# Optimization experiments

Measured on AMD Instinct MI355X. Metric: run time of the kernel, lower is better.

## Reference

```python
import jax, jax.numpy as jnp
import numpy as np

EMBED = 512
HEADS = 8
HIDDEN = 4 * EMBED
EPS = 1e-5


def setup_inputs() -> dict:
    key = jax.random.key(0)
    ks = jax.random.split(key, 12)
    s = lambda fan_in: 1.0 / np.sqrt(fan_in)
    return {
        "x": jax.random.normal(ks[0], (4, 2048, EMBED), dtype=jnp.float32),
        "ln1_g": jnp.ones((EMBED,), jnp.float32),
        "ln1_b": jnp.zeros((EMBED,), jnp.float32),
        "qkv_w": jax.random.uniform(ks[1], (EMBED, 3 * EMBED), jnp.float32, -s(EMBED), s(EMBED)),
        "qkv_b": jax.random.uniform(ks[2], (3 * EMBED,), jnp.float32, -s(EMBED), s(EMBED)),
        "proj_w": jax.random.uniform(ks[3], (EMBED, EMBED), jnp.float32, -s(EMBED), s(EMBED)),
        "proj_b": jax.random.uniform(ks[4], (EMBED,), jnp.float32, -s(EMBED), s(EMBED)),
        "ln2_g": jnp.ones((EMBED,), jnp.float32),
        "ln2_b": jnp.zeros((EMBED,), jnp.float32),
        "fc1_w": jax.random.uniform(ks[5], (EMBED, HIDDEN), jnp.float32, -s(EMBED), s(EMBED)),
        "fc1_b": jax.random.uniform(ks[6], (HIDDEN,), jnp.float32, -s(EMBED), s(EMBED)),
        "fc2_w": jax.random.uniform(ks[7], (HIDDEN, EMBED), jnp.float32, -s(HIDDEN), s(HIDDEN)),
        "fc2_b": jax.random.uniform(ks[8], (EMBED,), jnp.float32, -s(HIDDEN), s(HIDDEN)),
    }


def _layernorm(x, g, b):
    mu = jnp.mean(x, axis=-1, keepdims=True)
    var = jnp.mean(jnp.square(x - mu), axis=-1, keepdims=True)
    return (x - mu) * jax.lax.rsqrt(var + EPS) * g + b


def reference(x, ln1_g, ln1_b, qkv_w, qkv_b, proj_w, proj_b,
              ln2_g, ln2_b, fc1_w, fc1_b, fc2_w, fc2_b):
    B, N, C = x.shape
    H, D = HEADS, C // HEADS
    scale = D ** -0.5

    # --- attention sub-block (pre-LN) ---
    h = _layernorm(x, ln1_g, ln1_b)
    qkv = h @ qkv_w + qkv_b                      # [B,N,3C]
    q, k, v = jnp.split(qkv, 3, axis=-1)
    q = q.reshape(B, N, H, D).transpose(0, 2, 1, 3)  # [B,H,N,D]
    k = k.reshape(B, N, H, D).transpose(0, 2, 1, 3)
    v = v.reshape(B, N, H, D).transpose(0, 2, 1, 3)
    attn = jnp.einsum('bhqd,bhkd->bhqk', q, k) * scale
    attn = jax.nn.softmax(attn, axis=-1)
    o = jnp.einsum('bhqk,bhkd->bhqd', attn, v)
    o = o.transpose(0, 2, 1, 3).reshape(B, N, C)
    x = x + (o @ proj_w + proj_b)

    # --- MLP sub-block (pre-LN, exact GELU) ---
    h = _layernorm(x, ln2_g, ln2_b)
    h = jax.nn.gelu(h @ fc1_w + fc1_b, approximate=False)
    x = x + (h @ fc2_w + fc2_b)
    return x
```

## Files before the change

### kernel.cpp

```cpp
#include <hip/hip_runtime.h>
#include <math.h>


using bf16x8 = __attribute__((ext_vector_type(8))) short;
using f32x4  = __attribute__((ext_vector_type(4))) float;
using f32x16 = __attribute__((ext_vector_type(16))) float;

typedef unsigned short u16;
typedef unsigned int   u32;

__device__ __forceinline__ u16 f2bf(float f) {
    u32 u; __builtin_memcpy(&u, &f, 4);
    u32 r = u + 0x7FFFu + ((u >> 16) & 1u);
    return (u16)(r >> 16);
}
__device__ __forceinline__ u32 fbits(float f) {
    u32 u; __builtin_memcpy(&u, &f, 4); return u;
}
__device__ __forceinline__ float f_from_bits(u32 u) {
    float f; __builtin_memcpy(&f, &u, 4); return f;
}
__device__ __forceinline__ u32 pack_trunc(float lo, float hi) {
    return __builtin_amdgcn_perm(fbits(hi), fbits(lo), 0x07060302u);
}
__device__ __forceinline__ void gload16(const void* g, void* l) {
    __builtin_amdgcn_global_load_lds(
        (const __attribute__((address_space(1))) unsigned int*)g,
        (__attribute__((address_space(3))) unsigned int*)l, 16, 0, 0);
}

__global__ __launch_bounds__(256) void k_pre(
        const float* __restrict__ w0, u16* __restrict__ d0,
        const float* __restrict__ w1, u16* __restrict__ d1,
        const float* __restrict__ w2, u16* __restrict__ d2,
        const float* __restrict__ w3, u16* __restrict__ d3,
        const float* __restrict__ x, const float* __restrict__ g,
        const float* __restrict__ bta, u16* __restrict__ hout) {
    __shared__ float tile[32][33];
    const int bid = blockIdx.x;
    if (bid < 3072) {
        const float* w; u16* dst; int K, N, tb;
        if (bid < 768)       { w = w0; dst = d0; K = 512;  N = 1536; tb = bid; }
        else if (bid < 1024) { w = w1; dst = d1; K = 512;  N = 512;  tb = bid - 768; }
        else if (bid < 2048) { w = w2; dst = d2; K = 512;  N = 2048; tb = bid - 1024; }
        else                 { w = w3; dst = d3; K = 2048; N = 512;  tb = bid - 2048; }
        const int nb = N >> 5;
        const int k0 = (tb / nb) << 5;
        const int n0 = (tb % nb) << 5;
        const int c = threadIdx.x & 31, r = threadIdx.x >> 5;
#pragma unroll
        for (int i = 0; i < 4; i++)
            tile[r + i * 8][c] = w[(size_t)(k0 + r + i * 8) * N + n0 + c];
        __syncthreads();
#pragma unroll
        for (int i = 0; i < 4; i++)
            dst[(size_t)(n0 + r + i * 8) * K + k0 + c] = f2bf(tile[c][r + i * 8]);
    } else {
        const int row  = ((bid - 3072) << 2) + (threadIdx.x >> 6);
        const int lane = threadIdx.x & 63;
        const float* xr = x + (size_t)row * 512 + lane * 8;
        float4 a = *(const float4*)xr;
        float4 c = *(const float4*)(xr + 4);
        float s = a.x + a.y + a.z + a.w + c.x + c.y + c.z + c.w;
        float q = a.x*a.x + a.y*a.y + a.z*a.z + a.w*a.w
                + c.x*c.x + c.y*c.y + c.z*c.z + c.w*c.w;
#pragma unroll
        for (int off = 32; off; off >>= 1) {
            s += __shfl_xor(s, off, 64);
            q += __shfl_xor(q, off, 64);
        }
        const float mean = s * (1.0f / 512.0f);
        const float var  = q * (1.0f / 512.0f) - mean * mean;
        const float rstd = rsqrtf(var + 1e-5f);
        float vv[8] = {a.x, a.y, a.z, a.w, c.x, c.y, c.z, c.w};
#pragma unroll
        for (int j = 0; j < 8; j++) {
            const int col = lane * 8 + j;
            hout[(size_t)row * 512 + col] = f2bf((vv[j] - mean) * rstd * g[col] + bta[col]);
        }
    }
}

__global__ __launch_bounds__(256) void k_ln(const float* __restrict__ x,
                                            const float* __restrict__ g,
                                            const float* __restrict__ bta,
                                            u16* __restrict__ out) {
    const int row  = (blockIdx.x << 2) + (threadIdx.x >> 6);
    const int lane = threadIdx.x & 63;
    const float* xr = x + (size_t)row * 512 + lane * 8;
    float4 a = *(const float4*)xr;
    float4 c = *(const float4*)(xr + 4);
    float s = a.x + a.y + a.z + a.w + c.x + c.y + c.z + c.w;
    float q = a.x*a.x + a.y*a.y + a.z*a.z + a.w*a.w
            + c.x*c.x + c.y*c.y + c.z*c.z + c.w*c.w;
#pragma unroll
    for (int off = 32; off; off >>= 1) {
        s += __shfl_xor(s, off, 64);
        q += __shfl_xor(q, off, 64);
    }
    const float mean = s * (1.0f / 512.0f);
    const float var  = q * (1.0f / 512.0f) - mean * mean;
    const float rstd = rsqrtf(var + 1e-5f);
    float vv[8] = {a.x, a.y, a.z, a.w, c.x, c.y, c.z, c.w};
#pragma unroll
    for (int j = 0; j < 8; j++) {
        const int col = lane * 8 + j;
        out[(size_t)row * 512 + col] = f2bf((vv[j] - mean) * rstd * g[col] + bta[col]);
    }
}

template <int EP, int TN>
__global__ __launch_bounds__(256, 3) void k_gemm(const u16* __restrict__ A,
                                                 const u16* __restrict__ Bt,
                                                 const float* __restrict__ bias,
                                                 const float* __restrict__ res,
                                                 float* __restrict__ outF,
                                                 u16* __restrict__ outB,
                                                 u16* __restrict__ out2,
                                                 int M, int N, int K) {
    constexpr int NT = TN / 32;
    __shared__ u16 As[128 * 64];
    __shared__ u16 Bs[TN * 64];
    const int nb = N / TN;
    const int xg = blockIdx.x & 7, sg = blockIdx.x >> 3;
    const int m0 = ((sg / nb) * 8 + xg) << 7;
    const int n0 = (sg % nb) * TN;
    const int t = threadIdx.x, lane = t & 63, w = t >> 6;
    const int wr = (w >> 1) << 6;
    const int wc = (w & 1) * (TN / 2);
    const int quad = lane >> 4, l15 = lane & 15;
    const int x7 = l15 & 7;

    f32x4 acc[4][NT];
#pragma unroll
    for (int i = 0; i < 4; i++)
#pragma unroll
        for (int j = 0; j < NT; j++) acc[i][j] = (f32x4){0.f, 0.f, 0.f, 0.f};

    const size_t Kb = (size_t)K * 2;
    const char* ga = (const char*)A + (size_t)m0 * Kb;
    const char* gb = (const char*)Bt + (size_t)n0 * Kb;
    const int o0 = t * 16;

    for (int k0 = 0; k0 < K; k0 += 64) {
        const int kb = k0 * 2;
#pragma unroll
        for (int i = 0; i < 4; i++) {
            const int o4 = i * 4096 + o0;
            const int row = o4 >> 7;
            const int lc = ((o4 >> 4) & 7) ^ (row & 7);
            gload16(ga + (size_t)row * Kb + kb + lc * 16, (char*)As + o4);
        }
#pragma unroll
        for (int i = 0; i < TN / 32; i++) {
            const int o4 = i * 4096 + o0;
            const int row = o4 >> 7;
            const int lc = ((o4 >> 4) & 7) ^ (row & 7);
            gload16(gb + (size_t)row * Kb + kb + lc * 16, (char*)Bs + o4);
        }
        __syncthreads();
#pragma unroll
        for (int ks = 0; ks < 2; ks++) {
            const int cidx = ((ks * 4 + quad) ^ x7) * 8;
            bf16x8 af[4], bfr[NT];
#pragma unroll
            for (int i = 0; i < 4; i++)
                af[i] = *(const bf16x8*)(As + (wr + i * 16 + l15) * 64 + cidx);
#pragma unroll
            for (int j = 0; j < NT; j++)
                bfr[j] = *(const bf16x8*)(Bs + (wc + j * 16 + l15) * 64 + cidx);
#pragma unroll
            for (int mt = 0; mt < 4; mt++)
#pragma unroll
                for (int nt = 0; nt < NT; nt++)
                    acc[mt][nt] = __builtin_amdgcn_mfma_f32_16x16x32_bf16(
                        af[mt], bfr[nt], acc[mt][nt], 0, 0, 0);
        }
        __syncthreads();
    }

    const bool vpart = (EP == 3) && (n0 >= 1024);
    const bool qpart = (EP == 3) && (n0 < 512);
#pragma unroll
    for (int mt = 0; mt < 4; mt++)
#pragma unroll
        for (int nt = 0; nt < NT; nt++) {
            const int col = n0 + wc + nt * 16 + l15;
            const float bi = bias[col];
            const int row0 = m0 + wr + mt * 16 + quad * 4;
            if (vpart) {
                const int b = row0 >> 11, key = row0 & 2047;
                const int hd = col - 1024;
                u32 p0 = (u32)f2bf(acc[mt][nt][0] + bi) |
                         ((u32)f2bf(acc[mt][nt][1] + bi) << 16);
                u32 p1 = (u32)f2bf(acc[mt][nt][2] + bi) |
                         ((u32)f2bf(acc[mt][nt][3] + bi) << 16);
                *(uint2*)(out2 + (size_t)(b * 512 + hd) * 2048 + key) = make_uint2(p0, p1);
            } else {
#pragma unroll
                for (int r = 0; r < 4; r++) {
                    const int row = row0 + r;
                    float v = acc[mt][nt][r] + bi;
                    const size_t oi = (size_t)row * N + col;
                    if (EP == 1) {
                        float y = v * (0.79788456f + 0.035677408f * v * v);
                        y = fminf(y, 40.0f);
                        float tE = exp2f(y * 2.88539008f);
                        v = v * tE * __builtin_amdgcn_rcpf(tE + 1.0f);
                    }
                    if (qpart) v *= 0.18033688f;
                    if (EP == 2) outF[oi] = v + res[oi];
                    else         outB[oi] = f2bf(v);
                }
            }
        }
}

__global__ __launch_bounds__(256, 4) void k_attn(const u16* __restrict__ qkv,
                                                 const u16* __restrict__ vt,
                                                 u16* __restrict__ o) {
    __shared__ u16 smem[16384];
    const int bid = blockIdx.x;
    const int h = bid & 7, sg = bid >> 3;
    const int qt = sg & 15, b = sg >> 4;
    const int q0 = qt << 7;
    const int t = threadIdx.x, lane = t & 63, w = t >> 6;
    const int l31 = lane & 31, hi = lane >> 5;
    const int x7 = l31 & 7;

    char* sb = (char*)smem;
    const char* gk = (const char*)qkv + (size_t)(b << 11) * 3072 + 1024 + h * 128;
    const char* gv = (const char*)vt + (size_t)((b << 3) + h) * 64 * 4096;

#pragma unroll
    for (int i = 0; i < 2; i++) {
        const int o4 = i * 4096 + t * 16;
        const int row = o4 >> 7;
        const int lc = ((o4 >> 4) & 7) ^ (row & 7);
        gload16(gk + (size_t)row * 3072 + lc * 16, sb + o4);
        gload16(gv + (size_t)row * 4096 + lc * 16, sb + 8192 + o4);
    }

    bf16x8 qf[4];
    {
        const u16* gqp = qkv + (size_t)((b << 11) + q0 + w * 32 + l31) * 1536 + h * 64 + hi * 8;
#pragma unroll
        for (int ks = 0; ks < 4; ks++)
            qf[ks] = *(const bf16x8*)(gqp + ks * 16);
    }

    f32x16 accO[2];
#pragma unroll
    for (int i = 0; i < 16; i++) { accO[0][i] = 0.f; accO[1][i] = 0.f; }
    float dn = 0.f;

    for (int kt = 0; kt < 32; kt++) {
        const int cur = kt & 1;
        __syncthreads();
        if (kt < 31) {
            const int kk2 = (kt + 1) << 6;
            char* db = sb + (cur ^ 1) * 16384;
#pragma unroll
            for (int i = 0; i < 2; i++) {
                const int o4 = i * 4096 + t * 16;
                const int row = o4 >> 7;
                const int lc = ((o4 >> 4) & 7) ^ (row & 7);
                gload16(gk + (size_t)(kk2 + row) * 3072 + lc * 16, db + o4);
                gload16(gv + (size_t)row * 4096 + (size_t)kk2 * 2 + lc * 16, db + 8192 + o4);
            }
        }
        const u16* Ksc = smem + cur * 8192;
        const u16* Vsc = Ksc + 4096;

        f32x16 s2[2];
#pragma unroll
        for (int i = 0; i < 16; i++) { s2[0][i] = 0.f; s2[1][i] = 0.f; }
#pragma unroll
        for (int ks = 0; ks < 4; ks++) {
            const int cx = ((ks * 2 + hi) ^ x7) * 8;
            bf16x8 kf0 = *(const bf16x8*)(Ksc + l31 * 64 + cx);
            bf16x8 kf1 = *(const bf16x8*)(Ksc + (32 + l31) * 64 + cx);
            __builtin_amdgcn_s_setprio(1);
            s2[0] = __builtin_amdgcn_mfma_f32_32x32x16_bf16(kf0, qf[ks], s2[0], 0, 0, 0);
            s2[1] = __builtin_amdgcn_mfma_f32_32x32x16_bf16(kf1, qf[ks], s2[1], 0, 0, 0);
            __builtin_amdgcn_s_setprio(0);
        }

        u32 pfu[4][4];
#pragma unroll
        for (int mt = 0; mt < 2; mt++) {
            float pv[16];
#pragma unroll
            for (int r = 0; r < 16; r++) {
                pv[r] = __builtin_amdgcn_exp2f(s2[mt][r]);
                dn += pv[r];
            }
            u32 pk[4][2];
#pragma unroll
            for (int c = 0; c < 4; c++)
#pragma unroll
                for (int m = 0; m < 2; m++)
                    pk[c][m] = pack_trunc(pv[4 * c + 2 * m], pv[4 * c + 2 * m + 1]);
#pragma unroll
            for (int ksl = 0; ksl < 2; ksl++)
#pragma unroll
                for (int m = 0; m < 2; m++) {
                    auto rr = __builtin_amdgcn_permlane32_swap(
                        pk[ksl * 2][m], pk[ksl * 2 + 1][m], false, false);
                    pfu[mt * 2 + ksl][m]     = rr[0];
                    pfu[mt * 2 + ksl][m + 2] = rr[1];
                }
        }

#pragma unroll
        for (int ks = 0; ks < 4; ks++) {
            u32 pw[4] = {pfu[ks][0], pfu[ks][1], pfu[ks][2], pfu[ks][3]};
            bf16x8 pfv;
            __builtin_memcpy(&pfv, pw, 16);
            const int cx = ((ks * 2 + hi) ^ x7) * 8;
            bf16x8 vf0 = *(const bf16x8*)(Vsc + l31 * 64 + cx);
            bf16x8 vf1 = *(const bf16x8*)(Vsc + (32 + l31) * 64 + cx);
            __builtin_amdgcn_s_setprio(1);
            accO[0] = __builtin_amdgcn_mfma_f32_32x32x16_bf16(vf0, pfv, accO[0], 0, 0, 0);
            accO[1] = __builtin_amdgcn_mfma_f32_32x32x16_bf16(vf1, pfv, accO[1], 0, 0, 0);
            __builtin_amdgcn_s_setprio(0);
        }
    }

    dn += __shfl_xor(dn, 32, 64);
    const float rdn = __builtin_amdgcn_rcpf(dn);
    const int qg = q0 + w * 32 + l31;
#pragma unroll
    for (int mtd = 0; mtd < 2; mtd++)
#pragma unroll
        for (int g = 0; g < 4; g++) {
            const u32 p0 = (u32)f2bf(accO[mtd][4 * g + 0] * rdn) |
                           ((u32)f2bf(accO[mtd][4 * g + 1] * rdn) << 16);
            const u32 p1 = (u32)f2bf(accO[mtd][4 * g + 2] * rdn) |
                           ((u32)f2bf(accO[mtd][4 * g + 3] * rdn) << 16);
            const int d0 = mtd * 32 + g * 8 + hi * 4;
            *(uint2*)(o + (size_t)((b << 11) + qg) * 512 + h * 64 + d0) =
                make_uint2(p0, p1);
        }
}

extern "C" void kernel_launch(void* const* d_in, const int* in_sizes, int n_in,
                              void* d_out, int out_size, void* d_ws, size_t ws_size,
                              hipStream_t stream) {
    const float* x      = (const float*)d_in[0];
    const float* ln1_g  = (const float*)d_in[1];
    const float* ln1_b  = (const float*)d_in[2];
    const float* qkv_w  = (const float*)d_in[3];
    const float* qkv_b  = (const float*)d_in[4];
    const float* proj_w = (const float*)d_in[5];
    const float* proj_b = (const float*)d_in[6];
    const float* ln2_g  = (const float*)d_in[7];
    const float* ln2_b  = (const float*)d_in[8];
    const float* fc1_w  = (const float*)d_in[9];
    const float* fc1_b  = (const float*)d_in[10];
    const float* fc2_w  = (const float*)d_in[11];
    const float* fc2_b  = (const float*)d_in[12];
    float* out = (float*)d_out;
    char* ws = (char*)d_ws;

    u16*   qkv_wT = (u16*)(ws + 0);
    u16*   proj_wT= (u16*)(ws + 1572864);
    u16*   fc1_wT = (u16*)(ws + 2097152);
    u16*   fc2_wT = (u16*)(ws + 4194304);
    u16*   h      = (u16*)(ws + 6291456);
    u16*   qkv    = (u16*)(ws + 14680064);
    u16*   vt     = (u16*)(ws + 39845888);
    u16*   o      = (u16*)(ws + 48234496);
    float* x1     = (float*)(ws + 56623104);
    u16*   f1     = (u16*)(ws + 14680064);
    u16*   h2     = h;

    k_pre<<<5120, 256, 0, stream>>>(qkv_w, qkv_wT, proj_w, proj_wT,
                                    fc1_w, fc1_wT, fc2_w, fc2_wT,
                                    x, ln1_g, ln1_b, h);
    k_gemm<3,128><<<(8192/128)*(1536/128), 256, 0, stream>>>(
        h, qkv_wT, qkv_b, nullptr, nullptr, qkv, vt, 8192, 1536, 512);
    k_attn<<<512, 256, 0, stream>>>(qkv, vt, o);
    k_gemm<2,64><<<(8192/128)*(512/64), 256, 0, stream>>>(
        o, proj_wT, proj_b, x, x1, nullptr, nullptr, 8192, 512, 512);
    k_ln<<<2048, 256, 0, stream>>>(x1, ln2_g, ln2_b, h2);
    k_gemm<1,128><<<(8192/128)*(2048/128), 256, 0, stream>>>(
        h2, fc1_wT, fc1_b, nullptr, nullptr, f1, nullptr, 8192, 2048, 512);
    k_gemm<2,64><<<(8192/128)*(512/64), 256, 0, stream>>>(
        f1, fc2_wT, fc2_b, x1, out, nullptr, nullptr, 8192, 512, 2048);
}
```

Measured before the change: 234.3 us.

## Split attention KV sequence across two wave groups per block with LDS reduction

The attention kernel grows to 512 threads. Two groups of four waves each process alternating 64-key halves of a 128-key stage, so there are half as many loop iterations and twice as many waves to hide latency. At the end, the partial output accumulators and denominators are reduced through LDS before normalisation and store. The cost is twice the LDS buffer, an extra reduction phase with barriers, and possibly lower occupancy. The softmax appears to use no running max, so summing the partials needs no rescaling.

```diff
diff --git a/kernel.cpp b/kernel.cpp
--- a/kernel.cpp
+++ b/kernel.cpp
@@ -216,15 +216,16 @@
         }
 }
 
-__global__ __launch_bounds__(256, 4) void k_attn(const u16* __restrict__ qkv,
+__global__ __launch_bounds__(512, 4) void k_attn(const u16* __restrict__ qkv,
                                                  const u16* __restrict__ vt,
                                                  u16* __restrict__ o) {
-    __shared__ u16 smem[16384];
+    __shared__ u16 smem[32768];
     const int bid = blockIdx.x;
     const int h = bid & 7, sg = bid >> 3;
     const int qt = sg & 15, b = sg >> 4;
     const int q0 = qt << 7;
     const int t = threadIdx.x, lane = t & 63, w = t >> 6;
+    const int wq = w & 3, par = w >> 2;
     const int l31 = lane & 31, hi = lane >> 5;
     const int x7 = l31 & 7;
 
@@ -232,18 +233,21 @@
     const char* gk = (const char*)qkv + (size_t)(b << 11) * 3072 + 1024 + h * 128;
     const char* gv = (const char*)vt + (size_t)((b << 3) + h) * 64 * 4096;
 
-#pragma unroll
-    for (int i = 0; i < 2; i++) {
-        const int o4 = i * 4096 + t * 16;
-        const int row = o4 >> 7;
-        const int lc = ((o4 >> 4) & 7) ^ (row & 7);
-        gload16(gk + (size_t)row * 3072 + lc * 16, sb + o4);
-        gload16(gv + (size_t)row * 4096 + lc * 16, sb + 8192 + o4);
+    const int o4 = t * 16;
+    const int srow = o4 >> 7;
+    const int slc = ((o4 >> 4) & 7) ^ (srow & 7);
+
+    {
+        char* db = sb;
+        gload16(gk + (size_t)srow * 3072 + slc * 16,            db + o4);
+        gload16(gv + (size_t)srow * 4096 + slc * 16,            db + 8192 + o4);
+        gload16(gk + (size_t)(64 + srow) * 3072 + slc * 16,     db + 16384 + o4);
+        gload16(gv + (size_t)srow * 4096 + 128 + slc * 16,      db + 24576 + o4);
     }
 
     bf16x8 qf[4];
     {
-        const u16* gqp = qkv + (size_t)((b << 11) + q0 + w * 32 + l31) * 1536 + h * 64 + hi * 8;
+        const u16* gqp = qkv + (size_t)((b << 11) + q0 + wq * 32 + l31) * 1536 + h * 64 + hi * 8;
 #pragma unroll
         for (int ks = 0; ks < 4; ks++)
             qf[ks] = *(const bf16x8*)(gqp + ks * 16);
@@ -254,22 +258,18 @@
     for (int i = 0; i < 16; i++) { accO[0][i] = 0.f; accO[1][i] = 0.f; }
     float dn = 0.f;
 
-    for (int kt = 0; kt < 32; kt++) {
-        const int cur = kt & 1;
+    for (int st = 0; st < 16; st++) {
+        const int cur = st & 1;
         __syncthreads();
-        if (kt < 31) {
-            const int kk2 = (kt + 1) << 6;
-            char* db = sb + (cur ^ 1) * 16384;
-#pragma unroll
-            for (int i = 0; i < 2; i++) {
-                const int o4 = i * 4096 + t * 16;
-                const int row = o4 >> 7;
-                const int lc = ((o4 >> 4) & 7) ^ (row & 7);
-                gload16(gk + (size_t)(kk2 + row) * 3072 + lc * 16, db + o4);
-                gload16(gv + (size_t)row * 4096 + (size_t)kk2 * 2 + lc * 16, db + 8192 + o4);
-            }
-        }
-        const u16* Ksc = smem + cur * 8192;
+        if (st < 15) {
+            const int kkE = (st + 1) << 7;
+            char* db = sb + (cur ^ 1) * 32768;
+            gload16(gk + (size_t)(kkE + srow) * 3072 + slc * 16,       db + o4);
+            gload16(gv + (size_t)srow * 4096 + (size_t)kkE * 2 + slc * 16, db + 8192 + o4);
+            gload16(gk + (size_t)(kkE + 64 + srow) * 3072 + slc * 16,  db + 16384 + o4);
+            gload16(gv + (size_t)srow * 4096 + (size_t)(kkE + 64) * 2 + slc * 16, db + 24576 + o4);
+        }
+        const u16* Ksc = smem + cur * 16384 + par * 8192;
         const u16* Vsc = Ksc + 4096;
 
         f32x16 s2[2];
@@ -327,21 +327,46 @@
         }
     }
 
+    __syncthreads();
     dn += __shfl_xor(dn, 32, 64);
-    const float rdn = __builtin_amdgcn_rcpf(dn);
-    const int qg = q0 + w * 32 + l31;
-#pragma unroll
-    for (int mtd = 0; mtd < 2; mtd++)
-#pragma unroll
-        for (int g = 0; g < 4; g++) {
-            const u32 p0 = (u32)f2bf(accO[mtd][4 * g + 0] * rdn) |
-                           ((u32)f2bf(accO[mtd][4 * g + 1] * rdn) << 16);
-            const u32 p1 = (u32)f2bf(accO[mtd][4 * g + 2] * rdn) |
-                           ((u32)f2bf(accO[mtd][4 * g + 3] * rdn) << 16);
-            const int d0 = mtd * 32 + g * 8 + hi * 4;
-            *(uint2*)(o + (size_t)((b << 11) + qg) * 512 + h * 64 + d0) =
-                make_uint2(p0, p1);
-        }
+    {
+        char* base = sb + wq * 9216;
+        if (par) {
+#pragma unroll
+            for (int c = 0; c < 8; c++) {
+                f32x4 v4;
+#pragma unroll
+                for (int i = 0; i < 4; i++) v4[i] = accO[c >> 2][(c & 3) * 4 + i];
+                *(f32x4*)(base + (c * 64 + lane) * 16) = v4;
+            }
+            *(float*)(base + 8192 + lane * 4) = dn;
+        }
+        __syncthreads();
+        if (!par) {
+#pragma unroll
+            for (int c = 0; c < 8; c++) {
+                f32x4 v4 = *(const f32x4*)(base + (c * 64 + lane) * 16);
+#pragma unroll
+                for (int i = 0; i < 4; i++) accO[c >> 2][(c & 3) * 4 + i] += v4[i];
+            }
+            dn += *(const float*)(base + 8192 + lane * 4);
+
+            const float rdn = __builtin_amdgcn_rcpf(dn);
+            const int qg = q0 + wq * 32 + l31;
+#pragma unroll
+            for (int mtd = 0; mtd < 2; mtd++)
+#pragma unroll
+                for (int g = 0; g < 4; g++) {
+                    const u32 p0 = (u32)f2bf(accO[mtd][4 * g + 0] * rdn) |
+                                   ((u32)f2bf(accO[mtd][4 * g + 1] * rdn) << 16);
+                    const u32 p1 = (u32)f2bf(accO[mtd][4 * g + 2] * rdn) |
+                                   ((u32)f2bf(accO[mtd][4 * g + 3] * rdn) << 16);
+                    const int d0 = mtd * 32 + g * 8 + hi * 4;
+                    *(uint2*)(o + (size_t)((b << 11) + qg) * 512 + h * 64 + d0) =
+                        make_uint2(p0, p1);
+                }
+        }
+    }
 }
 
 extern "C" void kernel_launch(void* const* d_in, const int* in_sizes, int n_in,
@@ -380,7 +405,7 @@
                                     x, ln1_g, ln1_b, h);
     k_gemm<3,128><<<(8192/128)*(1536/128), 256, 0, stream>>>(
         h, qkv_wT, qkv_b, nullptr, nullptr, qkv, vt, 8192, 1536, 512);
-    k_attn<<<512, 256, 0, stream>>>(qkv, vt, o);
+    k_attn<<<512, 512, 0, stream>>>(qkv, vt, o);
     k_gemm<2,64><<<(8192/128)*(512/64), 256, 0, stream>>>(
         o, proj_wT, proj_b, x, x1, nullptr, nullptr, 8192, 512, 512);
     k_ln<<<2048, 256, 0, stream>>>(x1, ln2_g, ln2_b, h2);
```

Result: faster. 227.4 us (median of 2 runs) (-2.9%).
